# Kernel tuning notes

Hardware: AMD Instinct MI355X
Metric: run time of the kernel (lower is better)

## Reference

```python
import jax, jax.numpy as jnp
import numpy as np

N = 20000
E = 640000
H, C = 4, 64
L = 3
B = 16
EPS = 1e-5


def setup_inputs() -> dict:
    key = jax.random.key(0)
    ks = jax.random.split(key, 12)
    x = jax.random.normal(ks[0], (N, 256), dtype=jnp.float32)
    edge_index = jax.random.randint(ks[1], (2, E), 0, N, dtype=jnp.int64)
    batch = jnp.sort(jax.random.randint(ks[2], (N,), 0, B, dtype=jnp.int64))
    s = 0.05
    return {
        "x": x,
        "edge_index": edge_index,
        "batch": batch,
        "Wl": jax.random.normal(ks[3], (L, 256, H * C), dtype=jnp.float32) * s,
        "bl": jnp.zeros((L, H * C), dtype=jnp.float32),
        "Wr": jax.random.normal(ks[4], (L, 256, H * C), dtype=jnp.float32) * s,
        "br": jnp.zeros((L, H * C), dtype=jnp.float32),
        "att": jax.random.normal(ks[5], (L, H, C), dtype=jnp.float32) * s,
        "conv_bias": jnp.zeros((L, H * C), dtype=jnp.float32),
        "prelu_a": jnp.full((L,), 0.25, dtype=jnp.float32),
        "norm_w": jnp.ones((H * C,), dtype=jnp.float32),
        "norm_b": jnp.zeros((H * C,), dtype=jnp.float32),
        "norm_alpha": jnp.ones((H * C,), dtype=jnp.float32),
        "fc_W": jax.random.normal(ks[6], (H * C, 128), dtype=jnp.float32) * s,
        "fc_b": jnp.zeros((128,), dtype=jnp.float32),
    }


def graph_norm(h, w, b, alpha):
    # GraphNorm with batch=None: all rows form one segment (as in source forward)
    mean = jnp.mean(h, axis=0, keepdims=True)
    shifted = h - alpha * mean
    var = jnp.mean(shifted * shifted, axis=0, keepdims=True)
    return w * shifted / jnp.sqrt(var + EPS) + b


def gatv2_layer(h, src, dst, Wl, bl, Wr, br, att, bias):
    xl = (h @ Wl + bl).reshape(N, H, C)  # source transform
    xr = (h @ Wr + br).reshape(N, H, C)  # target transform
    m = jax.nn.leaky_relu(xl[src] + xr[dst], negative_slope=0.2)  # [Etot,H,C]
    e = jnp.einsum("ehc,hc->eh", m, att)  # [Etot,H]
    emax = jax.ops.segment_max(e, dst, num_segments=N)  # self-loops guarantee coverage
    ex = jnp.exp(e - emax[dst])
    denom = jax.ops.segment_sum(ex, dst, num_segments=N)
    alpha = ex / denom[dst]
    out = jax.ops.segment_sum(alpha[:, :, None] * xl[src], dst, num_segments=N)
    return out.reshape(N, H * C) + bias


def reference(x, edge_index, batch, Wl, bl, Wr, br, att, conv_bias, prelu_a,
              norm_w, norm_b, norm_alpha, fc_W, fc_b):
    loop = jnp.arange(N, dtype=edge_index.dtype)
    src = jnp.concatenate([edge_index[0], loop])  # add self-loops (PyG default)
    dst = jnp.concatenate([edge_index[1], loop])
    h = x
    for l in range(L):
        h = gatv2_layer(h, src, dst, Wl[l], bl[l], Wr[l], br[l], att[l], conv_bias[l])
        h = graph_norm(h, norm_w, norm_b, norm_alpha)
        h = jnp.where(h >= 0, h, prelu_a[l] * h)  # PReLU; dropout is identity in eval
    pooled = jax.ops.segment_sum(h, batch, num_segments=B)  # global_add_pool
    pooled = graph_norm(pooled, norm_w, norm_b, norm_alpha)  # shared norm reused after pool
    return pooled @ fc_W + fc_b
```

## Files before the change

kernel.cpp:

```cpp
#include <hip/hip_runtime.h>
#include <math.h>

#define N_NODES 20000
#define N_EDGES 640000
#define ETOT (N_EDGES + N_NODES)
#define HC 256
#define NLAYER 3
#define NBATCH 16
#define GEPS 1e-5f
#define NSLOT 64

typedef unsigned short u16;
typedef unsigned int u32;
typedef __attribute__((ext_vector_type(8))) short short8;
typedef __attribute__((ext_vector_type(4))) float floatx4;

__device__ __forceinline__ u16 f2bf(float f) {
    u32 u = __float_as_uint(f);
    u32 r = (u + 0x7FFFu + ((u >> 16) & 1u)) >> 16;
    return (u16)r;
}

__device__ __forceinline__ float4 bf2f4(uint2 u) {
    float4 r;
    r.x = __uint_as_float(u.x << 16);
    r.y = __uint_as_float(u.x & 0xFFFF0000u);
    r.z = __uint_as_float(u.y << 16);
    r.w = __uint_as_float(u.y & 0xFFFF0000u);
    return r;
}

__device__ __forceinline__ float dpp_red16(float x) {
    x += __int_as_float(__builtin_amdgcn_update_dpp(0, __float_as_int(x), 0xB1, 0xF, 0xF, true));
    x += __int_as_float(__builtin_amdgcn_update_dpp(0, __float_as_int(x), 0x4E, 0xF, 0xF, true));
    x += __int_as_float(__builtin_amdgcn_update_dpp(0, __float_as_int(x), 0x141, 0xF, 0xF, true));
    x += __int_as_float(__builtin_amdgcn_update_dpp(0, __float_as_int(x), 0x140, 0xF, 0xF, true));
    return x;
}


__global__ __launch_bounds__(256) void prep(const float* __restrict__ x, u16* __restrict__ xbf,
                                            const float* __restrict__ Wl, const float* __restrict__ Wr,
                                            u16* __restrict__ WT, uint4* __restrict__ zbase, int zq) {
    int b = blockIdx.x, tid = threadIdx.x;
    if (b < 1000) {
        for (int i = b * 256 + tid; i < 640000; i += 256000) {
            const float4* x4 = (const float4*)x + (size_t)i * 2;
            float4 a = x4[0], c = x4[1];
            u16 o[8] = {f2bf(a.x), f2bf(a.y), f2bf(a.z), f2bf(a.w),
                        f2bf(c.x), f2bf(c.y), f2bf(c.z), f2bf(c.w)};
            ((uint4*)xbf)[i] = *(const uint4*)o;
        }
    } else if (b < 1384) {
        __shared__ float T[32][33];
        int bi = b - 1000;
        int kb = bi & 7, nbk = (bi >> 3) & 15, l = bi >> 7;
        int n0 = nbk * 32, k0 = kb * 32;
        const float* W = ((n0 < 256) ? Wl : Wr) + (size_t)l * 65536;
        int nn = n0 & 255;
        int tx = tid & 31, ty = tid >> 5;
        #pragma unroll
        for (int i = 0; i < 4; ++i)
            T[ty + i * 8][tx] = W[(size_t)(k0 + ty + i * 8) * 256 + nn + tx];
        __syncthreads();
        u16* outw = WT + (size_t)l * 512 * 256;
        #pragma unroll
        for (int i = 0; i < 4; ++i)
            outw[(size_t)(n0 + ty + i * 8) * 256 + k0 + tx] = f2bf(T[tx][ty + i * 8]);
    } else {
        uint4 z = make_uint4(0, 0, 0, 0);
        for (int i = (b - 1384) * 256 + tid; i < zq; i += 120 * 256) zbase[i] = z;
    }
}


__global__ void count_deg(const int* __restrict__ dst, int* __restrict__ deg) {
    int e = blockIdx.x * 256 + threadIdx.x;
    if (e < N_EDGES) atomicAdd(&deg[dst[e]], 1);
}

__global__ __launch_bounds__(1024) void scan_excl(int* __restrict__ data, int* __restrict__ cursor) {
    __shared__ int wsum[16];
    int t = threadIdx.x, lane = t & 63, wid = t >> 6;
    int i0 = t * 20;
    int d[20];
    int tot = 0;
    #pragma unroll
    for (int j = 0; j < 20; ++j) {
        int i = i0 + j;
        int v = (i < N_NODES) ? (data[i] + 1) : 0;
        d[j] = v;
        tot += v;
    }
    int x = tot;
    #pragma unroll
    for (int off = 1; off < 64; off <<= 1) {
        int tmp = __shfl_up(x, off);
        if (lane >= off) x += tmp;
    }
    if (lane == 63) wsum[wid] = x;
    __syncthreads();
    if (t == 0) {
        int run = 0;
        #pragma unroll
        for (int w = 0; w < 16; ++w) { int tv = wsum[w]; wsum[w] = run; run += tv; }
    }
    __syncthreads();
    int run = wsum[wid] + x - tot;
    #pragma unroll
    for (int j = 0; j < 20; ++j) {
        int i = i0 + j;
        if (i < N_NODES) { data[i] = run; cursor[i] = run; }
        run += d[j];
    }
    if (t == 0) data[N_NODES] = ETOT;
}

__global__ void scatter_edges(const int* __restrict__ src, const int* __restrict__ dst,
                              int* __restrict__ cursor, int* __restrict__ col) {
    int t = blockIdx.x * 256 + threadIdx.x;
    if (t < N_NODES) {
        int p = atomicAdd(&cursor[t], 1);
        col[p] = t;
    } else if (t < N_NODES + N_EDGES) {
        int e = t - N_NODES;
        int p = atomicAdd(&cursor[dst[e]], 1);
        col[p] = src[e];
    }
}


__global__ __launch_bounds__(256) void gemm_mfma(
    const u16* __restrict__ Asrc, const float* __restrict__ slots_prev,
    const float* __restrict__ nw, const float* __restrict__ nb, const float* __restrict__ na,
    const float* __restrict__ pa, int prelu_idx, int use_norm,
    const u16* __restrict__ WT,
    const float* __restrict__ b0, const float* __restrict__ b1,
    u16* __restrict__ xlb, u16* __restrict__ xrb) {
    __shared__ u16 As[128][40];
    __shared__ u16 Bs[128][40];
    __shared__ float wcL[256], bbL[256];
    int row0 = blockIdx.x * 128;
    int nstrip = blockIdx.y;
    int ncol0 = nstrip * 128;
    const float* bias = (nstrip < 2) ? b0 : b1;
    u16* outp = (nstrip < 2) ? xlb : xrb;
    int c0 = (nstrip & 1) * 128;

    int tid = threadIdx.x;
    float ap = 0.f;
    if (use_norm) {
        int c = tid;
        float sum = 0.f, sq = 0.f;
        for (int s = 0; s < NSLOT; ++s) {
            sum += slots_prev[s * 512 + c];
            sq += slots_prev[s * 512 + 256 + c];
        }
        const float invn = 1.f / (float)N_NODES;
        float mean = sum * invn, Eh2 = sq * invn;
        float a = na[c];
        float var = Eh2 - (2.f * a - a * a) * mean * mean;
        float wc = nw[c] * rsqrtf(var + GEPS);
        wcL[c] = wc;
        bbL[c] = nb[c] - a * mean * wc;
        ap = pa[prelu_idx];
        __syncthreads();
    }

    int wave = tid >> 6, lane = tid & 63;
    int wm = (wave & 1) * 64, wn = (wave >> 1) * 64;
    int quad = lane >> 4, l16 = lane & 15;

    floatx4 acc[4][4] = {};

    int sr = tid >> 1;
    int sh = (tid & 1) * 16;

    for (int k0 = 0; k0 < 256; k0 += 32) {
        int gr = row0 + sr;
        uint4 av0 = make_uint4(0, 0, 0, 0), av1 = make_uint4(0, 0, 0, 0);
        if (gr < N_NODES) {
            const u16* p = Asrc + (size_t)gr * 256 + k0 + sh;
            av0 = *(const uint4*)p;
            av1 = *(const uint4*)(p + 8);
        }
        if (use_norm) {
            int kb2 = k0 + sh;
            u16 tmp[16];
            *(uint4*)tmp = av0;
            *(uint4*)(tmp + 8) = av1;
            float4 wv0 = *(const float4*)&wcL[kb2], wv1 = *(const float4*)&wcL[kb2 + 4];
            float4 wv2 = *(const float4*)&wcL[kb2 + 8], wv3 = *(const float4*)&wcL[kb2 + 12];
            float4 bv0 = *(const float4*)&bbL[kb2], bv1 = *(const float4*)&bbL[kb2 + 4];
            float4 bv2 = *(const float4*)&bbL[kb2 + 8], bv3 = *(const float4*)&bbL[kb2 + 12];
            float wvf[16] = {wv0.x, wv0.y, wv0.z, wv0.w, wv1.x, wv1.y, wv1.z, wv1.w,
                             wv2.x, wv2.y, wv2.z, wv2.w, wv3.x, wv3.y, wv3.z, wv3.w};
            float bvf[16] = {bv0.x, bv0.y, bv0.z, bv0.w, bv1.x, bv1.y, bv1.z, bv1.w,
                             bv2.x, bv2.y, bv2.z, bv2.w, bv3.x, bv3.y, bv3.z, bv3.w};
            u16 outv[16];
            #pragma unroll
            for (int j = 0; j < 16; ++j) {
                float vv = __uint_as_float(((u32)tmp[j]) << 16);
                float t2 = vv * wvf[j] + bvf[j];
                t2 = fmaxf(t2, ap * t2);
                outv[j] = f2bf(t2);
            }
            av0 = *(const uint4*)outv;
            av1 = *(const uint4*)(outv + 8);
        }
        const u16* q = WT + (size_t)(ncol0 + sr) * 256 + k0 + sh;
        uint4 bw0 = *(const uint4*)q;
        uint4 bw1 = *(const uint4*)(q + 8);
        *(uint4*)&As[sr][sh] = av0;
        *(uint4*)&As[sr][sh + 8] = av1;
        *(uint4*)&Bs[sr][sh] = bw0;
        *(uint4*)&Bs[sr][sh + 8] = bw1;
        __syncthreads();

        short8 af[4], bfr[4];
        #pragma unroll
        for (int mi = 0; mi < 4; ++mi)
            af[mi] = *(const short8*)&As[wm + mi * 16 + l16][quad * 8];
        #pragma unroll
        for (int ni = 0; ni < 4; ++ni)
            bfr[ni] = *(const short8*)&Bs[wn + ni * 16 + l16][quad * 8];
        #pragma unroll
        for (int mi = 0; mi < 4; ++mi)
            #pragma unroll
            for (int ni = 0; ni < 4; ++ni)
                acc[mi][ni] = __builtin_amdgcn_mfma_f32_16x16x32_bf16(af[mi], bfr[ni], acc[mi][ni], 0, 0, 0);
        __syncthreads();
    }

    #pragma unroll
    for (int ni = 0; ni < 4; ++ni) {
        int col = c0 + wn + ni * 16 + l16;
        float bv = bias[col];
        #pragma unroll
        for (int mi = 0; mi < 4; ++mi) {
            int gr = row0 + wm + mi * 16 + quad * 4;
            #pragma unroll
            for (int r = 0; r < 4; ++r) {
                if (gr + r < N_NODES)
                    outp[(size_t)(gr + r) * 256 + col] = f2bf(acc[mi][ni][r] + bv);
            }
        }
    }
}


__global__ __launch_bounds__(256) void gat_agg(
    const u16* __restrict__ xlb, const u16* __restrict__ xrb,
    const int* __restrict__ rowptr, const int* __restrict__ col,
    const float* __restrict__ att_l, const float* __restrict__ bias_l,
    u16* __restrict__ hB, float* __restrict__ slot) {
    __shared__ float sred[4][520];
    int wid = threadIdx.x >> 6, lane = threadIdx.x & 63;
    int node = blockIdx.x * 4 + wid;
    const uint2* xl2 = (const uint2*)xlb;
    float4 attv = ((const float4*)att_l)[lane];
    float4 xrv = bf2f4(((const uint2*)xrb)[(size_t)node * 64 + lane]);
    int beg = rowptr[node], end = rowptr[node + 1];

    float denom = 0.f;
    float4 acc = make_float4(0.f, 0.f, 0.f, 0.f);

    int j = beg;
    for (; j + 8 <= end; j += 8) {
        int s[8];
        uint2 raw[8];
        float4 a[8];
        float p[8];
        #pragma unroll
        for (int u = 0; u < 8; ++u) s[u] = col[j + u];
        #pragma unroll
        for (int u = 0; u < 8; ++u) raw[u] = xl2[(size_t)s[u] * 64 + lane];
        #pragma unroll
        for (int u = 0; u < 8; ++u) {
            a[u] = bf2f4(raw[u]);
            float vx = a[u].x + xrv.x, vy = a[u].y + xrv.y;
            float vz = a[u].z + xrv.z, vw = a[u].w + xrv.w;
            vx = fmaxf(vx, 0.2f * vx);
            vy = fmaxf(vy, 0.2f * vy);
            vz = fmaxf(vz, 0.2f * vz);
            vw = fmaxf(vw, 0.2f * vw);
            p[u] = vx * attv.x + vy * attv.y + vz * attv.z + vw * attv.w;
        }
        #pragma unroll
        for (int u = 0; u < 8; ++u) p[u] = dpp_red16(p[u]);
        #pragma unroll
        for (int u = 0; u < 8; ++u) {
            float w = __expf(p[u]);
            denom += w;
            acc.x += w * a[u].x; acc.y += w * a[u].y;
            acc.z += w * a[u].z; acc.w += w * a[u].w;
        }
    }
    for (; j < end; ++j) {
        int s = col[j];
        float4 a = bf2f4(xl2[(size_t)s * 64 + lane]);
        float vx = a.x + xrv.x, vy = a.y + xrv.y;
        float vz = a.z + xrv.z, vw = a.w + xrv.w;
        vx = fmaxf(vx, 0.2f * vx);
        vy = fmaxf(vy, 0.2f * vy);
        vz = fmaxf(vz, 0.2f * vz);
        vw = fmaxf(vw, 0.2f * vw);
        float p = vx * attv.x + vy * attv.y + vz * attv.z + vw * attv.w;
        p = dpp_red16(p);
        float w = __expf(p);
        denom += w;
        acc.x += w * a.x; acc.y += w * a.y; acc.z += w * a.z; acc.w += w * a.w;
    }

    float inv = 1.f / denom;
    float4 b4 = ((const float4*)bias_l)[lane];
    float4 o;
    o.x = acc.x * inv + b4.x; o.y = acc.y * inv + b4.y;
    o.z = acc.z * inv + b4.z; o.w = acc.w * inv + b4.w;
    u16 ob[4] = {f2bf(o.x), f2bf(o.y), f2bf(o.z), f2bf(o.w)};
    ((uint2*)hB)[(size_t)node * 64 + lane] = *(const uint2*)ob;

    int cb2 = lane * 4;
    sred[wid][cb2 + 0] = o.x; sred[wid][cb2 + 1] = o.y;
    sred[wid][cb2 + 2] = o.z; sred[wid][cb2 + 3] = o.w;
    sred[wid][256 + cb2 + 0] = o.x * o.x; sred[wid][256 + cb2 + 1] = o.y * o.y;
    sred[wid][256 + cb2 + 2] = o.z * o.z; sred[wid][256 + cb2 + 3] = o.w * o.w;
    __syncthreads();
    int t = threadIdx.x;
    #pragma unroll
    for (int h = 0; h < 2; ++h) {
        int idx = t + h * 256;
        float s = sred[0][idx] + sred[1][idx] + sred[2][idx] + sred[3][idx];
        atomicAdd(&slot[(blockIdx.x & (NSLOT - 1)) * 512 + idx], s);
    }
}


__global__ __launch_bounds__(256) void pool_kernel(const u16* __restrict__ hB,
                                                   const int* __restrict__ batch,
                                                   const float* __restrict__ slots2,
                                                   const float* __restrict__ nw, const float* __restrict__ nb,
                                                   const float* __restrict__ na, const float* __restrict__ pa,
                                                   float* __restrict__ pooled) {
    __shared__ float accs[NBATCH][256];
    int c = threadIdx.x;
    float sum = 0.f, sq = 0.f;
    for (int s = 0; s < NSLOT; ++s) {
        sum += slots2[s * 512 + c];
        sq += slots2[s * 512 + 256 + c];
    }
    const float invn = 1.f / (float)N_NODES;
    float mean = sum * invn, Eh2 = sq * invn;
    float a = na[c];
    float var = Eh2 - (2.f * a - a * a) * mean * mean;
    float wc = nw[c] * rsqrtf(var + GEPS);
    float bb = nb[c] - a * mean * wc;
    float ap = pa[2];

    #pragma unroll
    for (int b = 0; b < NBATCH; ++b) accs[b][c] = 0.f;
    int r0 = blockIdx.x * 100;
    int r1 = min(N_NODES, r0 + 100);
    for (int i = r0; i < r1; ++i) {
        float v = __uint_as_float(((u32)hB[(size_t)i * 256 + c]) << 16);
        v = v * wc + bb;
        v = fmaxf(v, ap * v);
        accs[batch[i]][c] += v;
    }
    int bmin = batch[r0], bmax = batch[r1 - 1];
    for (int b = bmin; b <= bmax; ++b) atomicAdd(&pooled[b * 256 + c], accs[b][c]);
}


__global__ __launch_bounds__(256) void pool_norm(const float* __restrict__ pooled,
                                                 const float* __restrict__ nw, const float* __restrict__ nb,
                                                 const float* __restrict__ na,
                                                 float* __restrict__ pn) {
    int c = threadIdx.x;
    float mean = 0.f, sq = 0.f;
    #pragma unroll
    for (int i = 0; i < NBATCH; ++i) {
        float v = pooled[i * 256 + c];
        mean += v; sq += v * v;
    }
    mean *= (1.f / NBATCH); sq *= (1.f / NBATCH);
    float a = na[c];
    float var = sq - (2.f * a - a * a) * mean * mean;
    float wc = nw[c] * rsqrtf(var + GEPS);
    float bb = nb[c] - a * mean * wc;
    #pragma unroll
    for (int i = 0; i < NBATCH; ++i)
        pn[i * 256 + c] = pooled[i * 256 + c] * wc + bb;
}


__global__ __launch_bounds__(256) void fc_kernel(const float* __restrict__ pn,
                                                 const float* __restrict__ fcW, const float* __restrict__ fcb,
                                                 float* __restrict__ out) {
    __shared__ float pnl[256];
    __shared__ float part[128];
    int b = blockIdx.x;
    int t = threadIdx.x;
    pnl[t] = pn[b * 256 + t];
    __syncthreads();
    int o = t & 127, half = t >> 7;
    float s = 0.f;
    int kbase = half * 128;
    #pragma unroll 8
    for (int k = 0; k < 128; ++k)
        s += pnl[kbase + k] * fcW[(kbase + k) * 128 + o];
    if (half == 1) part[o] = s;
    __syncthreads();
    if (half == 0) out[b * 128 + o] = s + part[o] + fcb[o];
}


extern "C" void kernel_launch(void* const* d_in, const int* in_sizes, int n_in,
                              void* d_out, int out_size, void* d_ws, size_t ws_size,
                              hipStream_t stream) {
    const float* x    = (const float*)d_in[0];
    const int*   ei   = (const int*)d_in[1];
    const int*   batch= (const int*)d_in[2];
    const float* Wl   = (const float*)d_in[3];
    const float* bl   = (const float*)d_in[4];
    const float* Wr   = (const float*)d_in[5];
    const float* br   = (const float*)d_in[6];
    const float* att  = (const float*)d_in[7];
    const float* cb   = (const float*)d_in[8];
    const float* pa   = (const float*)d_in[9];
    const float* nw   = (const float*)d_in[10];
    const float* nb   = (const float*)d_in[11];
    const float* na   = (const float*)d_in[12];
    const float* fcW  = (const float*)d_in[13];
    const float* fcb  = (const float*)d_in[14];
    float* out = (float*)d_out;

    char* ws = (char*)d_ws;
    size_t off = 0;
    auto carve = [&](size_t bytes) -> void* {
        void* p = (void*)(ws + off);
        off += (bytes + 255) & ~(size_t)255;
        return p;
    };
    size_t z0 = off;
    int*   rowptr = (int*)carve((N_NODES + 1) * sizeof(int));
    float* slots  = (float*)carve((size_t)NLAYER * NSLOT * 512 * sizeof(float));
    float* pooled = (float*)carve(NBATCH * HC * sizeof(float));
    size_t z1 = off;
    int*   cursor = (int*)carve(N_NODES * sizeof(int));
    int*   colidx = (int*)carve((size_t)ETOT * sizeof(int));
    u16*   xlb    = (u16*)carve((size_t)N_NODES * HC * sizeof(u16));
    u16*   xrb    = (u16*)carve((size_t)N_NODES * HC * sizeof(u16));
    u16*   hB     = (u16*)carve((size_t)N_NODES * HC * sizeof(u16));
    u16*   xbf    = (u16*)carve((size_t)N_NODES * HC * sizeof(u16));
    u16*   WT     = (u16*)carve((size_t)NLAYER * 512 * 256 * sizeof(u16));
    float* pn     = (float*)carve(NBATCH * HC * sizeof(float));

    int zq = (int)((z1 - z0) / 16);
    const int* srcp = ei;
    const int* dstp = ei + N_EDGES;

    prep<<<1504, 256, 0, stream>>>(x, xbf, Wl, Wr, WT, (uint4*)(ws + z0), zq);
    count_deg<<<(N_EDGES + 255) / 256, 256, 0, stream>>>(dstp, rowptr);
    scan_excl<<<1, 1024, 0, stream>>>(rowptr, cursor);
    scatter_edges<<<(ETOT + 255) / 256, 256, 0, stream>>>(srcp, dstp, cursor, colidx);

    for (int l = 0; l < NLAYER; ++l) {
        const u16* Asrc = (l == 0) ? xbf : hB;
        const float* slots_prev = slots + (size_t)((l > 0) ? (l - 1) : 0) * NSLOT * 512;
        gemm_mfma<<<dim3(157, 4), 256, 0, stream>>>(Asrc, slots_prev, nw, nb, na, pa,
                                                    (l > 0) ? (l - 1) : 0, (l > 0) ? 1 : 0,
                                                    WT + (size_t)l * 512 * 256,
                                                    bl + l * 256, br + l * 256, xlb, xrb);
        gat_agg<<<5000, 256, 0, stream>>>(xlb, xrb, rowptr, colidx, att + l * 256, cb + l * 256,
                                          hB, slots + (size_t)l * NSLOT * 512);
    }
    pool_kernel<<<200, 256, 0, stream>>>(hB, batch, slots + (size_t)2 * NSLOT * 512,
                                         nw, nb, na, pa, pooled);
    pool_norm<<<1, 256, 0, stream>>>(pooled, nw, nb, na, pn);
    fc_kernel<<<NBATCH, 256, 0, stream>>>(pn, fcW, fcb, out);
}
```

Measured before the change: 488.5 us.

## Split norm/PReLU out of GEMM, widen GEMM tile to 256 columns, use exp2

Moves the GraphNorm+PReLU transform out of the GEMM prologue into separate fin_stats and norm_prelu kernels. Before, each of the 4 column strips re-normalized its A tile; now a normalized bf16 copy is written once per layer. The GEMM tile widens to 128x256, so each block covers a full xl or xr output with half the blocks and half the A reloads. Attention logits are pre-scaled by log2(e) so exp2f replaces __expf. This adds two launches and an extra full read/write of the hidden state per layer, and the wider tile raises register pressure.

Measured after the change: 601.6 us. 1.23x slower.

```diff
diff --git a/kernel.cpp b/kernel.cpp
--- a/kernel.cpp
+++ b/kernel.cpp
@@ -9,6 +9,7 @@
 #define NBATCH 16
 #define GEPS 1e-5f
 #define NSLOT 64
+#define L2E 1.44269504f
 
 typedef unsigned short u16;
 typedef unsigned int u32;
@@ -131,110 +132,66 @@
 
 
 __global__ __launch_bounds__(256) void gemm_mfma(
-    const u16* __restrict__ Asrc, const float* __restrict__ slots_prev,
-    const float* __restrict__ nw, const float* __restrict__ nb, const float* __restrict__ na,
-    const float* __restrict__ pa, int prelu_idx, int use_norm,
-    const u16* __restrict__ WT,
+    const u16* __restrict__ Abf, const u16* __restrict__ WTl,
     const float* __restrict__ b0, const float* __restrict__ b1,
     u16* __restrict__ xlb, u16* __restrict__ xrb) {
     __shared__ u16 As[128][40];
-    __shared__ u16 Bs[128][40];
-    __shared__ float wcL[256], bbL[256];
+    __shared__ u16 Bs[256][40];
     int row0 = blockIdx.x * 128;
     int nstrip = blockIdx.y;
-    int ncol0 = nstrip * 128;
-    const float* bias = (nstrip < 2) ? b0 : b1;
-    u16* outp = (nstrip < 2) ? xlb : xrb;
-    int c0 = (nstrip & 1) * 128;
+    const float* bias = nstrip ? b1 : b0;
+    u16* outp = nstrip ? xrb : xlb;
+    const u16* Wbase = WTl + (size_t)nstrip * 256 * 256;
 
     int tid = threadIdx.x;
-    float ap = 0.f;
-    if (use_norm) {
-        int c = tid;
-        float sum = 0.f, sq = 0.f;
-        for (int s = 0; s < NSLOT; ++s) {
-            sum += slots_prev[s * 512 + c];
-            sq += slots_prev[s * 512 + 256 + c];
-        }
-        const float invn = 1.f / (float)N_NODES;
-        float mean = sum * invn, Eh2 = sq * invn;
-        float a = na[c];
-        float var = Eh2 - (2.f * a - a * a) * mean * mean;
-        float wc = nw[c] * rsqrtf(var + GEPS);
-        wcL[c] = wc;
-        bbL[c] = nb[c] - a * mean * wc;
-        ap = pa[prelu_idx];
-        __syncthreads();
-    }
-
     int wave = tid >> 6, lane = tid & 63;
-    int wm = (wave & 1) * 64, wn = (wave >> 1) * 64;
+    int wm = (wave & 1) * 64, wn = (wave >> 1) * 128;
     int quad = lane >> 4, l16 = lane & 15;
 
-    floatx4 acc[4][4] = {};
-
-    int sr = tid >> 1;
-    int sh = (tid & 1) * 16;
+    floatx4 acc[4][8] = {};
+
+    int sra = tid >> 1;
+    int sha = (tid & 1) * 16;
 
     for (int k0 = 0; k0 < 256; k0 += 32) {
-        int gr = row0 + sr;
-        uint4 av0 = make_uint4(0, 0, 0, 0), av1 = make_uint4(0, 0, 0, 0);
+        int gr = row0 + sra;
+        uint4 av0 = make_uint4(0, 0, 0, 0), av1 = av0;
         if (gr < N_NODES) {
-            const u16* p = Asrc + (size_t)gr * 256 + k0 + sh;
+            const u16* p = Abf + (size_t)gr * 256 + k0 + sha;
             av0 = *(const uint4*)p;
             av1 = *(const uint4*)(p + 8);
         }
-        if (use_norm) {
-            int kb2 = k0 + sh;
-            u16 tmp[16];
-            *(uint4*)tmp = av0;
-            *(uint4*)(tmp + 8) = av1;
-            float4 wv0 = *(const float4*)&wcL[kb2], wv1 = *(const float4*)&wcL[kb2 + 4];
-            float4 wv2 = *(const float4*)&wcL[kb2 + 8], wv3 = *(const float4*)&wcL[kb2 + 12];
-            float4 bv0 = *(const float4*)&bbL[kb2], bv1 = *(const float4*)&bbL[kb2 + 4];
-            float4 bv2 = *(const float4*)&bbL[kb2 + 8], bv3 = *(const float4*)&bbL[kb2 + 12];
-            float wvf[16] = {wv0.x, wv0.y, wv0.z, wv0.w, wv1.x, wv1.y, wv1.z, wv1.w,
-                             wv2.x, wv2.y, wv2.z, wv2.w, wv3.x, wv3.y, wv3.z, wv3.w};
-            float bvf[16] = {bv0.x, bv0.y, bv0.z, bv0.w, bv1.x, bv1.y, bv1.z, bv1.w,
-                             bv2.x, bv2.y, bv2.z, bv2.w, bv3.x, bv3.y, bv3.z, bv3.w};
-            u16 outv[16];
-            #pragma unroll
-            for (int j = 0; j < 16; ++j) {
-                float vv = __uint_as_float(((u32)tmp[j]) << 16);
-                float t2 = vv * wvf[j] + bvf[j];
-                t2 = fmaxf(t2, ap * t2);
-                outv[j] = f2bf(t2);
-            }
-            av0 = *(const uint4*)outv;
-            av1 = *(const uint4*)(outv + 8);
-        }
-        const u16* q = WT + (size_t)(ncol0 + sr) * 256 + k0 + sh;
-        uint4 bw0 = *(const uint4*)q;
-        uint4 bw1 = *(const uint4*)(q + 8);
-        *(uint4*)&As[sr][sh] = av0;
-        *(uint4*)&As[sr][sh + 8] = av1;
-        *(uint4*)&Bs[sr][sh] = bw0;
-        *(uint4*)&Bs[sr][sh + 8] = bw1;
+        const u16* q = Wbase + (size_t)tid * 256 + k0;
+        uint4 bv0 = *(const uint4*)q;
+        uint4 bv1 = *(const uint4*)(q + 8);
+        uint4 bv2 = *(const uint4*)(q + 16);
+        uint4 bv3 = *(const uint4*)(q + 24);
+        *(uint4*)&As[sra][sha] = av0;
+        *(uint4*)&As[sra][sha + 8] = av1;
+        *(uint4*)&Bs[tid][0] = bv0;
+        *(uint4*)&Bs[tid][8] = bv1;
+        *(uint4*)&Bs[tid][16] = bv2;
+        *(uint4*)&Bs[tid][24] = bv3;
         __syncthreads();
 
-        short8 af[4], bfr[4];
+        short8 af[4], bfr[8];
         #pragma unroll
         for (int mi = 0; mi < 4; ++mi)
             af[mi] = *(const short8*)&As[wm + mi * 16 + l16][quad * 8];
         #pragma unroll
-        for (int ni = 0; ni < 4; ++ni)
+        for (int ni = 0; ni < 8; ++ni)
             bfr[ni] = *(const short8*)&Bs[wn + ni * 16 + l16][quad * 8];
         #pragma unroll
         for (int mi = 0; mi < 4; ++mi)
             #pragma unroll
-            for (int ni = 0; ni < 4; ++ni)
+            for (int ni = 0; ni < 8; ++ni)
                 acc[mi][ni] = __builtin_amdgcn_mfma_f32_16x16x32_bf16(af[mi], bfr[ni], acc[mi][ni], 0, 0, 0);
         __syncthreads();
     }
 
     #pragma unroll
-    for (int ni = 0; ni < 4; ++ni) {
-        int col = c0 + wn + ni * 16 + l16;
+    for (int ni = 0; ni < 8; ++ni) {
+        int col = wn + ni * 16 + l16;
         float bv = bias[col];
         #pragma unroll
         for (int mi = 0; mi < 4; ++mi) {
@@ -259,6 +216,7 @@
     int node = blockIdx.x * 4 + wid;
     const uint2* xl2 = (const uint2*)xlb;
     float4 attv = ((const float4*)att_l)[lane];
+    attv.x *= L2E; attv.y *= L2E; attv.z *= L2E; attv.w *= L2E;
     float4 xrv = bf2f4(((const uint2*)xrb)[(size_t)node * 64 + lane]);
     int beg = rowptr[node], end = rowptr[node + 1];
 
@@ -290,7 +248,7 @@
         for (int u = 0; u < 8; ++u) p[u] = dpp_red16(p[u]);
         #pragma unroll
         for (int u = 0; u < 8; ++u) {
-            float w = __expf(p[u]);
+            float w = exp2f(p[u]);
             denom += w;
             acc.x += w * a[u].x; acc.y += w * a[u].y;
             acc.z += w * a[u].z; acc.w += w * a[u].w;
@@ -307,7 +265,7 @@
         vw = fmaxf(vw, 0.2f * vw);
         float p = vx * attv.x + vy * attv.y + vz * attv.z + vw * attv.w;
         p = dpp_red16(p);
-        float w = __expf(p);
+        float w = exp2f(p);
         denom += w;
         acc.x += w * a.x; acc.y += w * a.y; acc.z += w * a.z; acc.w += w * a.w;
     }
@@ -333,6 +291,54 @@
         float s = sred[0][idx] + sred[1][idx] + sred[2][idx] + sred[3][idx];
         atomicAdd(&slot[(blockIdx.x & (NSLOT - 1)) * 512 + idx], s);
     }
+}
+
+
+__global__ __launch_bounds__(256) void fin_stats(const float* __restrict__ slot,
+                                                 const float* __restrict__ nw, const float* __restrict__ nb,
+                                                 const float* __restrict__ na,
+                                                 float* __restrict__ wcbb) {
+    int c = threadIdx.x;
+    float sum = 0.f, sq = 0.f;
+    for (int s = 0; s < NSLOT; ++s) {
+        sum += slot[s * 512 + c];
+        sq += slot[s * 512 + 256 + c];
+    }
+    const float invn = 1.f / (float)N_NODES;
+    float mean = sum * invn, Eh2 = sq * invn;
+    float a = na[c];
+    float var = Eh2 - (2.f * a - a * a) * mean * mean;
+    float wc = nw[c] * rsqrtf(var + GEPS);
+    wcbb[c] = wc;
+    wcbb[256 + c] = nb[c] - a * mean * wc;
+}
+
+
+__global__ __launch_bounds__(256) void norm_prelu(const u16* __restrict__ hB, u16* __restrict__ hbf,
+                                                  const float* __restrict__ wcbb,
+                                                  const float* __restrict__ pa, int l) {
+    int t = threadIdx.x;
+    int row = blockIdx.x * 8 + (t >> 5);
+    int c = (t & 31) * 8;
+    float ap = pa[l];
+    float4 wc0 = *(const float4*)&wcbb[c];
+    float4 wc1 = *(const float4*)&wcbb[c + 4];
+    float4 bb0 = *(const float4*)&wcbb[256 + c];
+    float4 bb1 = *(const float4*)&wcbb[256 + c + 4];
+    uint4 raw = ((const uint4*)hB)[(size_t)row * 32 + (c >> 3)];
+    float4 a = bf2f4(make_uint2(raw.x, raw.y));
+    float4 b = bf2f4(make_uint2(raw.z, raw.w));
+    a.x = a.x * wc0.x + bb0.x; a.y = a.y * wc0.y + bb0.y;
+    a.z = a.z * wc0.z + bb0.z; a.w = a.w * wc0.w + bb0.w;
+    b.x = b.x * wc1.x + bb1.x; b.y = b.y * wc1.y + bb1.y;
+    b.z = b.z * wc1.z + bb1.z; b.w = b.w * wc1.w + bb1.w;
+    a.x = fmaxf(a.x, ap * a.x); a.y = fmaxf(a.y, ap * a.y);
+    a.z = fmaxf(a.z, ap * a.z); a.w = fmaxf(a.w, ap * a.w);
+    b.x = fmaxf(b.x, ap * b.x); b.y = fmaxf(b.y, ap * b.y);
+    b.z = fmaxf(b.z, ap * b.z); b.w = fmaxf(b.w, ap * b.w);
+    u16 o[8] = {f2bf(a.x), f2bf(a.y), f2bf(a.z), f2bf(a.w),
+                f2bf(b.x), f2bf(b.y), f2bf(b.z), f2bf(b.w)};
+    ((uint4*)hbf)[(size_t)row * 32 + (c >> 3)] = *(const uint4*)o;
 }
 
 
@@ -453,7 +459,9 @@
     u16*   xrb    = (u16*)carve((size_t)N_NODES * HC * sizeof(u16));
     u16*   hB     = (u16*)carve((size_t)N_NODES * HC * sizeof(u16));
     u16*   xbf    = (u16*)carve((size_t)N_NODES * HC * sizeof(u16));
+    u16*   hbf    = (u16*)carve((size_t)N_NODES * HC * sizeof(u16));
     u16*   WT     = (u16*)carve((size_t)NLAYER * 512 * 256 * sizeof(u16));
+    float* wcbb   = (float*)carve(512 * sizeof(float));
     float* pn     = (float*)carve(NBATCH * HC * sizeof(float));
 
     int zq = (int)((z1 - z0) / 16);
@@ -466,14 +474,15 @@
     scatter_edges<<<(ETOT + 255) / 256, 256, 0, stream>>>(srcp, dstp, cursor, colidx);
 
     for (int l = 0; l < NLAYER; ++l) {
-        const u16* Asrc = (l == 0) ? xbf : hB;
-        const float* slots_prev = slots + (size_t)((l > 0) ? (l - 1) : 0) * NSLOT * 512;
-        gemm_mfma<<<dim3(157, 4), 256, 0, stream>>>(Asrc, slots_prev, nw, nb, na, pa,
-                                                    (l > 0) ? (l - 1) : 0, (l > 0) ? 1 : 0,
-                                                    WT + (size_t)l * 512 * 256,
+        const u16* Asrc = (l == 0) ? xbf : hbf;
+        gemm_mfma<<<dim3(157, 2), 256, 0, stream>>>(Asrc, WT + (size_t)l * 512 * 256,
                                                     bl + l * 256, br + l * 256, xlb, xrb);
         gat_agg<<<5000, 256, 0, stream>>>(xlb, xrb, rowptr, colidx, att + l * 256, cb + l * 256,
                                           hB, slots + (size_t)l * NSLOT * 512);
+        if (l < NLAYER - 1) {
+            fin_stats<<<1, 256, 0, stream>>>(slots + (size_t)l * NSLOT * 512, nw, nb, na, wcbb);
+            norm_prelu<<<2500, 256, 0, stream>>>(hB, hbf, wcbb, pa, l);
+        }
     }
     pool_kernel<<<200, 256, 0, stream>>>(hB, batch, slots + (size_t)2 * NSLOT * 512,
                                          nw, nb, na, pa, pooled);
```
